# Performance work log

Measured on AMD Instinct MI355X. Metric: run time of the kernel, lower is better.

## Reference

```python
import jax, jax.numpy as jnp
import numpy as np

NUM_HEADS = 16
GRID_SIZE = 16


def rotate(x, pos):
    # x: [B, nH, N, D] with D even; pos: [N] float
    D = x.shape[-1]
    half = D // 2
    omega = jnp.arange(half, dtype=x.dtype) / half
    omega = 1.0 / (10000.0 ** omega)
    freq = pos[:, None].astype(x.dtype) * omega          # [N, half]
    # torch .repeat(1,1,1,2) TILES the last dim (not interleave)
    emb_sin = jnp.tile(jnp.sin(freq), (1, 2))            # [N, D]
    emb_cos = jnp.tile(jnp.cos(freq), (1, 2))
    y = x.reshape(x.shape[:-1] + (half, 2))
    rot = jnp.stack((-y[..., 1], y[..., 0]), axis=-1).reshape(x.shape)
    return x * emb_cos + rot * emb_sin


def setup_inputs() -> dict:
    key = jax.random.key(0)
    k1, k2, k3, k4 = jax.random.split(key, 4)
    B, N, C = 2, 2048, 1024
    return {
        "x": jax.random.normal(k1, (B, N, C), dtype=jnp.float32),
        "W_qkv": jax.random.normal(k2, (3 * C, C), dtype=jnp.float32) * 0.02,
        "W_proj": jax.random.normal(k3, (C, C), dtype=jnp.float32) * 0.02,
        "b_proj": jax.random.normal(k4, (C,), dtype=jnp.float32) * 0.02,
        "T": 8,
        "H": 16,
        "W": 16,
    }


def reference(x, W_qkv, W_proj, b_proj, T, H, W):
    B, N, C = x.shape
    nH = NUM_HEADS
    hd = C // nH
    d_dim = 2 * (hd // 3 // 2)   # 20 for hd=64
    h_dim = d_dim
    w_dim = d_dim

    # axial positions (mask=None path): ids = arange(T*H*W)
    ids = jnp.arange(T * H * W)
    d_pos = (ids // (H * W)).astype(jnp.float32)
    rem = ids % (H * W)
    h_pos = (rem // W).astype(jnp.float32) * (GRID_SIZE / H)
    w_pos = (rem % W).astype(jnp.float32) * (GRID_SIZE / W)

    # fused QKV projection (no bias)
    qkv = jnp.einsum('bnc,oc->bno', x, W_qkv)            # [B, N, 3C]
    qkv = qkv.reshape(B, N, 3, nH, hd).transpose(2, 0, 3, 1, 4)
    q, k, v = qkv[0], qkv[1], qkv[2]                     # [B, nH, N, hd]

    s0, s1, s2 = 0, d_dim, d_dim + h_dim
    s3 = s2 + w_dim
    qd = rotate(q[..., s0:s1], d_pos); kd = rotate(k[..., s0:s1], d_pos)
    qh = rotate(q[..., s1:s2], h_pos); kh = rotate(k[..., s1:s2], h_pos)
    qw = rotate(q[..., s2:s3], w_pos); kw = rotate(k[..., s2:s3], w_pos)
    if s3 < hd:
        q = jnp.concatenate([qd, qh, qw, q[..., s3:]], axis=-1)
        k = jnp.concatenate([kd, kh, kw, k[..., s3:]], axis=-1)
    else:
        q = jnp.concatenate([qd, qh, qw], axis=-1)
        k = jnp.concatenate([kd, kh, kw], axis=-1)

    # SDPA (default scale = hd**-0.5, no dropout, not causal)
    scale = hd ** (-0.5)
    scores = jnp.einsum('bhqd,bhkd->bhqk', q, k) * scale
    attn = jax.nn.softmax(scores, axis=-1)
    out = jnp.einsum('bhqk,bhkd->bhqd', attn, v)          # [B, nH, N, hd]

    out = out.transpose(0, 2, 1, 3).reshape(B, N, C)
    out = jnp.einsum('bnc,oc->bno', out, W_proj) + b_proj
    return out


if __name__ == "__main__":
    inp = setup_inputs()
    y = reference(**inp)
    print(y.shape, y.dtype)
```

## Files before the change

kernel.cpp:

```cpp
#include <hip/hip_runtime.h>
#include <stdint.h>

typedef unsigned short u16;
typedef __attribute__((ext_vector_type(8))) short bf16x8;
typedef __attribute__((ext_vector_type(4))) float f32x4;

#define DEVI static __device__ __forceinline__

static constexpr int NTOK = 2048;
static constexpr int CDIM = 1024;
static constexpr int C3   = 3072;

DEVI u16 f2bf(float f) {
  uint32_t u = __float_as_uint(f);
  return (u16)((u + 0x7fffu + ((u >> 16) & 1u)) >> 16);
}

DEVI float exp2fast(float x) { return __builtin_amdgcn_exp2f(x); }

DEVI void gl_lds16(const void* g, void* l) {
  __builtin_amdgcn_global_load_lds(
      (__attribute__((address_space(1))) uint32_t*)g,
      (__attribute__((address_space(3))) uint32_t*)l, 16, 0, 0);
}

DEVI f32x4 mfma16(bf16x8 a, bf16x8 b, f32x4 c) {
  return __builtin_amdgcn_mfma_f32_16x16x32_bf16(a, b, c, 0, 0, 0);
}

__global__ void k_cvt3(const float* __restrict__ x, const float* __restrict__ wq,
                       const float* __restrict__ wp, u16* __restrict__ xb,
                       u16* __restrict__ wqb, u16* __restrict__ wpb) {
  int i = (blockIdx.x * blockDim.x + threadIdx.x) * 4;
  const float* src; u16* dst; int off;
  if (i < 4194304)      { src = x;  dst = xb;  off = i; }
  else if (i < 7340032) { src = wq; dst = wqb; off = i - 4194304; }
  else                  { src = wp; dst = wpb; off = i - 7340032; }
  float4 v = *reinterpret_cast<const float4*>(src + off);
  ushort4 o;
  o.x = f2bf(v.x); o.y = f2bf(v.y); o.z = f2bf(v.z); o.w = f2bf(v.w);
  *reinterpret_cast<ushort4*>(dst + off) = o;
}

template<int MODE>
__global__ __launch_bounds__(256, 2) void k_gemm(
    const u16* __restrict__ A, const u16* __restrict__ Bw,
    float* __restrict__ Cout, const float* __restrict__ bias,
    u16* __restrict__ qb, u16* __restrict__ kb, u16* __restrict__ vT,
    int Nn, int K) {
  __shared__ u16 smem[MODE == 2 ? 17408 : 8192];
  u16* Al = smem;
  u16* Bl = smem + 4096;
  const int tid = threadIdx.x, wid = tid >> 6, lane = tid & 63;
  const int bm = blockIdx.x, bn = blockIdx.y;
  const int wr = wid >> 1, wc = wid & 1;
  const int fr = lane & 15, fg = lane >> 4;
  f32x4 acc[4][4] = {};

  const int r0 = wid * 16 + (lane >> 2);
  const int c0 = (lane & 3) * 8;
  const u16* Ag = A + (size_t)(bm * 128) * K + c0;
  const u16* Bg = Bw + (size_t)(bn * 128) * K + c0;
  u16* Alb = Al + wid * 512;
  u16* Blb = Bl + wid * 512;
  const int fk = fg * 8;

  for (int kt = 0; kt < K; kt += 32) {
    __syncthreads();
    gl_lds16(Ag + (size_t)r0 * K + kt,        Alb);
    gl_lds16(Ag + (size_t)(64 + r0) * K + kt, Alb + 2048);
    gl_lds16(Bg + (size_t)r0 * K + kt,        Blb);
    gl_lds16(Bg + (size_t)(64 + r0) * K + kt, Blb + 2048);
    __syncthreads();
    bf16x8 af[4], bfr[4];
#pragma unroll
    for (int i = 0; i < 4; ++i)
      af[i] = *reinterpret_cast<const bf16x8*>(&Al[(wr * 64 + i * 16 + fr) * 32 + fk]);
#pragma unroll
    for (int j = 0; j < 4; ++j)
      bfr[j] = *reinterpret_cast<const bf16x8*>(&Bl[(wc * 64 + j * 16 + fr) * 32 + fk]);
#pragma unroll
    for (int i = 0; i < 4; ++i)
#pragma unroll
      for (int j = 0; j < 4; ++j)
        acc[i][j] = mfma16(af[i], bfr[j], acc[i][j]);
  }
  const int orow0 = bm * 128 + wr * 64 + fg * 4;

  if constexpr (MODE == 1) {
    const int ocol0 = bn * 128 + wc * 64 + fr;
#pragma unroll
    for (int j = 0; j < 4; ++j) {
      int col = ocol0 + j * 16;
      float badd = bias[col];
#pragma unroll
      for (int i = 0; i < 4; ++i)
#pragma unroll
        for (int r = 0; r < 4; ++r)
          Cout[(size_t)(orow0 + i * 16 + r) * Nn + col] = acc[i][j][r] + badd;
    }
  } else {
    const int which = bn >> 3;
    if (which < 2) {
      const int cbase = (bn & 7) * 128 + wc * 64 + fr;
      u16* dst = (which == 0) ? qb : kb;
#pragma unroll
      for (int j = 0; j < 4; ++j) {
        const int c = cbase + j * 16;
        const int d = c & 63, hh = c >> 6;
        const bool dorope = (d < 60);
        int seg = 0; float omega = 0.f;
        if (dorope) {
          seg = d / 20;
          int ds = d - seg * 20;
          int jj = (ds >= 10) ? ds - 10 : ds;
          omega = exp2fast(-1.3287712379549449f * (float)jj);
        }
#pragma unroll
        for (int i = 0; i < 4; ++i) {
#pragma unroll
          for (int r = 0; r < 4; ++r) {
            const int m = orow0 + i * 16 + r;
            const int b = m >> 11, n = m & (NTOK - 1);
            float val = acc[i][j][r];
            float pr = __shfl_xor(val, 1, 64);
            float outv = val;
            if (dorope) {
              float pos = (seg == 0) ? (float)(n >> 8)
                        : (seg == 1) ? (float)((n >> 4) & 15)
                                     : (float)(n & 15);
              float f = pos * omega, sn, cs;
              __sincosf(f, &sn, &cs);
              outv = (d & 1) ? val * cs + pr * sn : val * cs - pr * sn;
            }
            if (which == 0) outv *= 0.18033688011112042f;
            dst[((size_t)(b * 16 + hh) * NTOK + n) * 64 + d] = f2bf(outv);
          }
        }
      }
    } else {
      __syncthreads();
      const int mbase = wr * 64 + fg * 4;
#pragma unroll
      for (int j = 0; j < 4; ++j) {
        const int crow = wc * 64 + j * 16 + fr;
#pragma unroll
        for (int i = 0; i < 4; ++i) {
          ushort4 pk;
          pk.x = f2bf(acc[i][j][0]); pk.y = f2bf(acc[i][j][1]);
          pk.z = f2bf(acc[i][j][2]); pk.w = f2bf(acc[i][j][3]);
          *reinterpret_cast<ushort4*>(&smem[crow * 136 + mbase + i * 16]) = pk;
        }
      }
      __syncthreads();
      const int c = tid >> 1, mh = (tid & 1) * 64;
      const int cfull = (bn & 7) * 128 + c;
      const int hh = cfull >> 6, d = cfull & 63;
      const int b = bm >> 4;
      u16* dst = vT + (((size_t)(b * 16 + hh)) * 64 + d) * NTOK + (bm & 15) * 128 + mh;
      const u16* srcl = &smem[c * 136 + mh];
#pragma unroll
      for (int s = 0; s < 8; ++s)
        *reinterpret_cast<bf16x8*>(dst + s * 8) = *reinterpret_cast<const bf16x8*>(srcl + s * 8);
    }
  }
}

__global__ __launch_bounds__(256, 4) void k_attn(
    const u16* __restrict__ qb, const u16* __restrict__ kb,
    const u16* __restrict__ vT, u16* __restrict__ outb) {
  __shared__ u16 Kl[2][64 * 64];
  __shared__ u16 Vl[2][64 * 64];
  __shared__ u16 Pl[4][16 * 64];
  const int bh = blockIdx.x;
  const int qt = blockIdx.y;
  const int tid = threadIdx.x, wid = tid >> 6, lane = tid & 63;
  const int fr = lane & 15, fg = lane >> 4;
  const int swz = fr & 7;

  bf16x8 qf[2];
  const u16* qbase = qb + ((size_t)bh * NTOK + qt * 64 + wid * 16 + fr) * 64;
#pragma unroll
  for (int h = 0; h < 2; ++h)
    qf[h] = *reinterpret_cast<const bf16x8*>(qbase + h * 32 + fg * 8);

  f32x4 acc[4] = {};
  float mrun = -1e30f, lrun = 0.f;

  const int srow = lane >> 3;
  const int scol = ((lane & 7) ^ srow) * 8;
  const u16* kg = kb + ((size_t)bh * NTOK + wid * 8 + srow) * 64 + scol;
  const u16* vg = vT + ((size_t)bh * 64 + wid * 8 + srow) * NTOK + scol;
  u16* Pw = &Pl[wid][0];

  auto stage = [&](int buf, int kvt) {
#pragma unroll
    for (int s = 0; s < 2; ++s) {
      gl_lds16(kg + (size_t)(kvt + s * 32) * 64, &Kl[buf][s * 2048 + wid * 512]);
      gl_lds16(vg + (size_t)(s * 32) * NTOK + kvt, &Vl[buf][s * 2048 + wid * 512]);
    }
  };

  stage(0, 0);
  __syncthreads();
  int cur = 0;
  for (int kvt = 0; kvt < NTOK; kvt += 64) {
    if (kvt + 64 < NTOK) stage(cur ^ 1, kvt + 64);
    const u16* Kc = &Kl[cur][0];
    const u16* Vc = &Vl[cur][0];

    bf16x8 kf[4][2], vf[4][2];
#pragma unroll
    for (int mf = 0; mf < 4; ++mf) {
      int rb = (mf * 16 + fr) * 64;
#pragma unroll
      for (int h = 0; h < 2; ++h)
        kf[mf][h] = *reinterpret_cast<const bf16x8*>(Kc + rb + (((h * 4 + fg) ^ swz) * 8));
    }
#pragma unroll
    for (int nf = 0; nf < 4; ++nf) {
      int rb = (nf * 16 + fr) * 64;
#pragma unroll
      for (int ks = 0; ks < 2; ++ks)
        vf[nf][ks] = *reinterpret_cast<const bf16x8*>(Vc + rb + (((ks * 4 + fg) ^ swz) * 8));
    }

    f32x4 st[4];
    __builtin_amdgcn_s_setprio(1);
#pragma unroll
    for (int mf = 0; mf < 4; ++mf) {
      f32x4 s0 = {};
      s0 = mfma16(kf[mf][0], qf[0], s0);
      s0 = mfma16(kf[mf][1], qf[1], s0);
      st[mf] = s0;
    }
    __builtin_amdgcn_s_setprio(0);

    float t0 = fmaxf(fmaxf(st[0][0], st[0][1]), fmaxf(st[0][2], st[0][3]));
    float t1 = fmaxf(fmaxf(st[1][0], st[1][1]), fmaxf(st[1][2], st[1][3]));
    float t2 = fmaxf(fmaxf(st[2][0], st[2][1]), fmaxf(st[2][2], st[2][3]));
    float t3 = fmaxf(fmaxf(st[3][0], st[3][1]), fmaxf(st[3][2], st[3][3]));
    float tm = fmaxf(fmaxf(t0, t1), fmaxf(t2, t3));
    tm = fmaxf(tm, __shfl_xor(tm, 16, 64));
    tm = fmaxf(tm, __shfl_xor(tm, 32, 64));
    bool skip = (__all(tm - mrun <= 8.f) != 0);
    float corr, mref;
    if (skip) {
      corr = 1.f; mref = mrun;
    } else {
      float mnew = fmaxf(mrun, tm);
      corr = exp2fast(mrun - mnew);
      mrun = mnew; mref = mnew;
    }
    float ps = 0.f;
#pragma unroll
    for (int mf = 0; mf < 4; ++mf) {
      float p0 = exp2fast(st[mf][0] - mref);
      float p1 = exp2fast(st[mf][1] - mref);
      float p2 = exp2fast(st[mf][2] - mref);
      float p3 = exp2fast(st[mf][3] - mref);
      ps += (p0 + p1) + (p2 + p3);
      uint32_t k0, k1;
      asm("v_cvt_pk_bf16_f32 %0, %1, %2" : "=v"(k0) : "v"(p0), "v"(p1));
      asm("v_cvt_pk_bf16_f32 %0, %1, %2" : "=v"(k1) : "v"(p2), "v"(p3));
      int c16 = (mf * 2 + (fg >> 1)) ^ swz;
      uint2 val; val.x = k0; val.y = k1;
      *reinterpret_cast<uint2*>(Pw + fr * 64 + c16 * 8 + (fg & 1) * 4) = val;
    }
    ps += __shfl_xor(ps, 16, 64);
    ps += __shfl_xor(ps, 32, 64);
    lrun = lrun * corr + ps;

    asm volatile("" ::: "memory");

    if (!skip) {
      float cr[4];
#pragma unroll
      for (int r = 0; r < 4; ++r) cr[r] = __shfl(corr, fg * 4 + r, 64);
#pragma unroll
      for (int nf = 0; nf < 4; ++nf)
#pragma unroll
        for (int r = 0; r < 4; ++r) acc[nf][r] *= cr[r];
    }
    bf16x8 pa[2];
#pragma unroll
    for (int ks = 0; ks < 2; ++ks)
      pa[ks] = *reinterpret_cast<const bf16x8*>(Pw + fr * 64 + (((ks * 4 + fg) ^ swz) * 8));
    __builtin_amdgcn_s_setprio(1);
#pragma unroll
    for (int nf = 0; nf < 4; ++nf)
#pragma unroll
      for (int ks = 0; ks < 2; ++ks)
        acc[nf] = mfma16(pa[ks], vf[nf][ks], acc[nf]);
    __builtin_amdgcn_s_setprio(0);

    __syncthreads();
    cur ^= 1;
  }

  const int b = bh >> 4, h = bh & 15;
  float linv[4];
#pragma unroll
  for (int r = 0; r < 4; ++r) linv[r] = 1.f / __shfl(lrun, fg * 4 + r, 64);
#pragma unroll
  for (int nf = 0; nf < 4; ++nf)
#pragma unroll
    for (int r = 0; r < 4; ++r) {
      int n = qt * 64 + wid * 16 + fg * 4 + r;
      int col = h * 64 + nf * 16 + fr;
      outb[((size_t)b * NTOK + n) * CDIM + col] = f2bf(acc[nf][r] * linv[r]);
    }
}

extern "C" void kernel_launch(void* const* d_in, const int* in_sizes, int n_in,
                              void* d_out, int out_size, void* d_ws, size_t ws_size,
                              hipStream_t stream) {
  (void)in_sizes; (void)n_in; (void)out_size; (void)ws_size;
  const float* x  = (const float*)d_in[0];
  const float* Wq = (const float*)d_in[1];
  const float* Wp = (const float*)d_in[2];
  const float* bp = (const float*)d_in[3];

  char* w = (char*)d_ws;
  u16* x_bf  = (u16*)(w + 0);
  u16* wq_bf = (u16*)(w + 8388608);
  u16* wp_bf = (u16*)(w + 14680064);
  u16* q_bf  = (u16*)(w + 16777216);
  u16* k_bf  = (u16*)(w + 25165824);
  u16* vT    = (u16*)(w + 33554432);
  u16* at_bf = (u16*)(w + 41943040);

  k_cvt3<<<8192, 256, 0, stream>>>(x, Wq, Wp, x_bf, wq_bf, wp_bf);

  k_gemm<2><<<dim3(32, 24), 256, 0, stream>>>(x_bf, wq_bf, nullptr, nullptr,
                                              q_bf, k_bf, vT, C3, CDIM);

  k_attn<<<dim3(32, 32), 256, 0, stream>>>(q_bf, k_bf, vT, at_bf);

  k_gemm<1><<<dim3(32, 8), 256, 0, stream>>>(at_bf, wp_bf, (float*)d_out, bp,
                                             nullptr, nullptr, nullptr, CDIM, CDIM);
}
```

Before: 134.7 us.

## Switch attention to 32x32x16 MFMA with register-resident P via permlane swaps

Rewrites the attention kernel to use 32x32x16 bf16 MFMA tiles, so each wave handles 32 query rows and each block 128 queries, halving the grid along the query axis. The P matrix is no longer written to and read back from LDS; it is rearranged in registers with permlane32_swap to form the A operand of the PV product. K and V fragments are loaded from LDS inside the MFMA loops instead of being preloaded. The larger accumulators raise register pressure (launch bounds drop to 2 blocks per CU), and the halved grid gives fewer blocks to spread across CUs.

After: 121.5 us. 1.11x faster.

```diff
diff --git a/kernel.cpp b/kernel.cpp
--- a/kernel.cpp
+++ b/kernel.cpp
@@ -4,6 +4,8 @@
 typedef unsigned short u16;
 typedef __attribute__((ext_vector_type(8))) short bf16x8;
 typedef __attribute__((ext_vector_type(4))) float f32x4;
+typedef __attribute__((ext_vector_type(16))) float f32x16;
+typedef __attribute__((ext_vector_type(2))) unsigned int u32x2;
 
 #define DEVI static __device__ __forceinline__
 
@@ -26,6 +28,9 @@
 
 DEVI f32x4 mfma16(bf16x8 a, bf16x8 b, f32x4 c) {
   return __builtin_amdgcn_mfma_f32_16x16x32_bf16(a, b, c, 0, 0, 0);
+}
+DEVI f32x16 mfma32(bf16x8 a, bf16x8 b, f32x16 c) {
+  return __builtin_amdgcn_mfma_f32_32x32x16_bf16(a, b, c, 0, 0, 0);
 }
 
 __global__ void k_cvt3(const float* __restrict__ x, const float* __restrict__ wq,
@@ -166,32 +171,30 @@
   }
 }
 
-__global__ __launch_bounds__(256, 4) void k_attn(
-    const u16* __restrict__ qb, const u16* __restrict__ kb,
-    const u16* __restrict__ vT, u16* __restrict__ outb) {
+__global__ __launch_bounds__(256, 2) void k_attn(
+    const u16* __restrict__ qp, const u16* __restrict__ kp,
+    const u16* __restrict__ vp, u16* __restrict__ op) {
   __shared__ u16 Kl[2][64 * 64];
   __shared__ u16 Vl[2][64 * 64];
-  __shared__ u16 Pl[4][16 * 64];
   const int bh = blockIdx.x;
   const int qt = blockIdx.y;
   const int tid = threadIdx.x, wid = tid >> 6, lane = tid & 63;
-  const int fr = lane & 15, fg = lane >> 4;
-  const int swz = fr & 7;
-
-  bf16x8 qf[2];
-  const u16* qbase = qb + ((size_t)bh * NTOK + qt * 64 + wid * 16 + fr) * 64;
-#pragma unroll
-  for (int h = 0; h < 2; ++h)
-    qf[h] = *reinterpret_cast<const bf16x8*>(qbase + h * 32 + fg * 8);
-
-  f32x4 acc[4] = {};
+  const int lo = lane & 31, hi = lane >> 5;
+
+  const int q0 = qt * 128 + wid * 32;
+  const u16* qrow = qp + ((size_t)bh * NTOK + q0 + lo) * 64 + hi * 8;
+  bf16x8 qf[4];
+#pragma unroll
+  for (int c = 0; c < 4; ++c)
+    qf[c] = *reinterpret_cast<const bf16x8*>(qrow + c * 16);
+
+  f32x16 acc2[2] = {};
   float mrun = -1e30f, lrun = 0.f;
 
   const int srow = lane >> 3;
   const int scol = ((lane & 7) ^ srow) * 8;
-  const u16* kg = kb + ((size_t)bh * NTOK + wid * 8 + srow) * 64 + scol;
-  const u16* vg = vT + ((size_t)bh * 64 + wid * 8 + srow) * NTOK + scol;
-  u16* Pw = &Pl[wid][0];
+  const u16* kg = kp + ((size_t)bh * NTOK + wid * 8 + srow) * 64 + scol;
+  const u16* vg = vp + ((size_t)bh * 64 + wid * 8 + srow) * NTOK + scol;
 
   auto stage = [&](int buf, int kvt) {
 #pragma unroll
@@ -209,39 +212,28 @@
     const u16* Kc = &Kl[cur][0];
     const u16* Vc = &Vl[cur][0];
 
-    bf16x8 kf[4][2], vf[4][2];
-#pragma unroll
-    for (int mf = 0; mf < 4; ++mf) {
-      int rb = (mf * 16 + fr) * 64;
-#pragma unroll
-      for (int h = 0; h < 2; ++h)
-        kf[mf][h] = *reinterpret_cast<const bf16x8*>(Kc + rb + (((h * 4 + fg) ^ swz) * 8));
-    }
-#pragma unroll
-    for (int nf = 0; nf < 4; ++nf) {
-      int rb = (nf * 16 + fr) * 64;
-#pragma unroll
-      for (int ks = 0; ks < 2; ++ks)
-        vf[nf][ks] = *reinterpret_cast<const bf16x8*>(Vc + rb + (((ks * 4 + fg) ^ swz) * 8));
-    }
-
-    f32x4 st[4];
+    f32x16 st2[2];
     __builtin_amdgcn_s_setprio(1);
 #pragma unroll
-    for (int mf = 0; mf < 4; ++mf) {
-      f32x4 s0 = {};
-      s0 = mfma16(kf[mf][0], qf[0], s0);
-      s0 = mfma16(kf[mf][1], qf[1], s0);
-      st[mf] = s0;
+    for (int mt = 0; mt < 2; ++mt) {
+      f32x16 s = {};
+      const int rr = mt * 32 + lo;
+      const int rb = rr * 64;
+#pragma unroll
+      for (int c = 0; c < 4; ++c) {
+        bf16x8 kf = *reinterpret_cast<const bf16x8*>(Kc + rb + (((c * 2 + hi) ^ (rr & 7)) * 8));
+        s = mfma32(kf, qf[c], s);
+      }
+      st2[mt] = s;
     }
     __builtin_amdgcn_s_setprio(0);
 
-    float t0 = fmaxf(fmaxf(st[0][0], st[0][1]), fmaxf(st[0][2], st[0][3]));
-    float t1 = fmaxf(fmaxf(st[1][0], st[1][1]), fmaxf(st[1][2], st[1][3]));
-    float t2 = fmaxf(fmaxf(st[2][0], st[2][1]), fmaxf(st[2][2], st[2][3]));
-    float t3 = fmaxf(fmaxf(st[3][0], st[3][1]), fmaxf(st[3][2], st[3][3]));
-    float tm = fmaxf(fmaxf(t0, t1), fmaxf(t2, t3));
-    tm = fmaxf(tm, __shfl_xor(tm, 16, 64));
+    float tp[4] = {-1e30f, -1e30f, -1e30f, -1e30f};
+#pragma unroll
+    for (int mt = 0; mt < 2; ++mt)
+#pragma unroll
+      for (int r = 0; r < 16; ++r) tp[r & 3] = fmaxf(tp[r & 3], st2[mt][r]);
+    float tm = fmaxf(fmaxf(tp[0], tp[1]), fmaxf(tp[2], tp[3]));
     tm = fmaxf(tm, __shfl_xor(tm, 32, 64));
     bool skip = (__all(tm - mrun <= 8.f) != 0);
     float corr, mref;
@@ -252,46 +244,56 @@
       corr = exp2fast(mrun - mnew);
       mrun = mnew; mref = mnew;
     }
-    float ps = 0.f;
-#pragma unroll
-    for (int mf = 0; mf < 4; ++mf) {
-      float p0 = exp2fast(st[mf][0] - mref);
-      float p1 = exp2fast(st[mf][1] - mref);
-      float p2 = exp2fast(st[mf][2] - mref);
-      float p3 = exp2fast(st[mf][3] - mref);
-      ps += (p0 + p1) + (p2 + p3);
-      uint32_t k0, k1;
-      asm("v_cvt_pk_bf16_f32 %0, %1, %2" : "=v"(k0) : "v"(p0), "v"(p1));
-      asm("v_cvt_pk_bf16_f32 %0, %1, %2" : "=v"(k1) : "v"(p2), "v"(p3));
-      int c16 = (mf * 2 + (fg >> 1)) ^ swz;
-      uint2 val; val.x = k0; val.y = k1;
-      *reinterpret_cast<uint2*>(Pw + fr * 64 + c16 * 8 + (fg & 1) * 4) = val;
-    }
-    ps += __shfl_xor(ps, 16, 64);
+    float psp[4] = {0.f, 0.f, 0.f, 0.f};
+    uint32_t pk[2][8];
+#pragma unroll
+    for (int mt = 0; mt < 2; ++mt)
+#pragma unroll
+      for (int jj = 0; jj < 8; ++jj) {
+        float p0 = exp2fast(st2[mt][2 * jj]     - mref);
+        float p1 = exp2fast(st2[mt][2 * jj + 1] - mref);
+        psp[jj & 3] += p0 + p1;
+        uint32_t w;
+        asm("v_cvt_pk_bf16_f32 %0, %1, %2" : "=v"(w) : "v"(p0), "v"(p1));
+        pk[mt][jj] = w;
+      }
+    float ps = (psp[0] + psp[1]) + (psp[2] + psp[3]);
     ps += __shfl_xor(ps, 32, 64);
     lrun = lrun * corr + ps;
 
-    asm volatile("" ::: "memory");
+    bf16x8 pa[4];
+#pragma unroll
+    for (int ks = 0; ks < 4; ++ks) {
+      const int mt = ks >> 1, g = (ks & 1) * 4;
+      u32x2 sA = __builtin_amdgcn_permlane32_swap(pk[mt][g + 0], pk[mt][g + 2], false, false);
+      u32x2 sB = __builtin_amdgcn_permlane32_swap(pk[mt][g + 1], pk[mt][g + 3], false, false);
+      union { uint32_t u[4]; bf16x8 v; } x;
+      x.u[0] = sA[0]; x.u[1] = sB[0]; x.u[2] = sA[1]; x.u[3] = sB[1];
+      pa[ks] = x.v;
+    }
 
     if (!skip) {
-      float cr[4];
-#pragma unroll
-      for (int r = 0; r < 4; ++r) cr[r] = __shfl(corr, fg * 4 + r, 64);
-#pragma unroll
-      for (int nf = 0; nf < 4; ++nf)
-#pragma unroll
-        for (int r = 0; r < 4; ++r) acc[nf][r] *= cr[r];
-    }
-    bf16x8 pa[2];
-#pragma unroll
-    for (int ks = 0; ks < 2; ++ks)
-      pa[ks] = *reinterpret_cast<const bf16x8*>(Pw + fr * 64 + (((ks * 4 + fg) ^ swz) * 8));
+      float cr[16];
+#pragma unroll
+      for (int r = 0; r < 16; ++r)
+        cr[r] = __shfl(corr, (r & 3) + 8 * (r >> 2) + 4 * hi, 64);
+#pragma unroll
+      for (int nf = 0; nf < 2; ++nf)
+#pragma unroll
+        for (int r = 0; r < 16; ++r) acc2[nf][r] *= cr[r];
+    }
+
     __builtin_amdgcn_s_setprio(1);
 #pragma unroll
-    for (int nf = 0; nf < 4; ++nf)
-#pragma unroll
-      for (int ks = 0; ks < 2; ++ks)
-        acc[nf] = mfma16(pa[ks], vf[nf][ks], acc[nf]);
+    for (int nf = 0; nf < 2; ++nf) {
+      const int rr = nf * 32 + lo;
+      const int rb = rr * 64;
+#pragma unroll
+      for (int ks = 0; ks < 4; ++ks) {
+        bf16x8 vf = *reinterpret_cast<const bf16x8*>(Vc + rb + (((ks * 2 + hi) ^ (rr & 7)) * 8));
+        acc2[nf] = mfma32(pa[ks], vf, acc2[nf]);
+      }
+    }
     __builtin_amdgcn_s_setprio(0);
 
     __syncthreads();
@@ -299,16 +301,17 @@
   }
 
   const int b = bh >> 4, h = bh & 15;
-  float linv[4];
-#pragma unroll
-  for (int r = 0; r < 4; ++r) linv[r] = 1.f / __shfl(lrun, fg * 4 + r, 64);
-#pragma unroll
-  for (int nf = 0; nf < 4; ++nf)
-#pragma unroll
-    for (int r = 0; r < 4; ++r) {
-      int n = qt * 64 + wid * 16 + fg * 4 + r;
-      int col = h * 64 + nf * 16 + fr;
-      outb[((size_t)b * NTOK + n) * CDIM + col] = f2bf(acc[nf][r] * linv[r]);
+  float linv[16];
+#pragma unroll
+  for (int r = 0; r < 16; ++r)
+    linv[r] = 1.f / __shfl(lrun, (r & 3) + 8 * (r >> 2) + 4 * hi, 64);
+#pragma unroll
+  for (int nf = 0; nf < 2; ++nf)
+#pragma unroll
+    for (int r = 0; r < 16; ++r) {
+      int n = q0 + (r & 3) + 8 * (r >> 2) + 4 * hi;
+      int col = h * 64 + nf * 32 + lo;
+      op[((size_t)b * NTOK + n) * CDIM + col] = f2bf(acc2[nf][r] * linv[r]);
     }
 }
 
@@ -335,7 +338,7 @@
   k_gemm<2><<<dim3(32, 24), 256, 0, stream>>>(x_bf, wq_bf, nullptr, nullptr,
                                               q_bf, k_bf, vT, C3, CDIM);
 
-  k_attn<<<dim3(32, 32), 256, 0, stream>>>(q_bf, k_bf, vT, at_bf);
+  k_attn<<<dim3(32, 16), 256, 0, stream>>>(q_bf, k_bf, vT, at_bf);
 
   k_gemm<1><<<dim3(32, 8), 256, 0, stream>>>(at_bf, wp_bf, (float*)d_out, bp,
                                              nullptr, nullptr, nullptr, CDIM, CDIM);
```
